# Kernel tuning notes

Hardware: AMD Instinct MI355X
Metric: run time of the kernel (lower is better)

The kernel has to match this reference:

```python
import jax, jax.numpy as jnp
import numpy as np

B, S, D = 4, 4096, 2048  # batch, seq, hidden
E, R, K = 8, 16, 2       # n_experts, rank, top_k


def setup_inputs() -> dict:
    key = jax.random.key(0)
    k1, k2, k3, k4 = jax.random.split(key, 4)
    x = jax.random.normal(k1, (B, S, D), dtype=jnp.float32)
    router_w = jax.random.normal(k2, (E, D), dtype=jnp.float32) * 0.02  # nn.Linear weight (out,in)
    experts_down = jax.random.normal(k3, (E, D, R), dtype=jnp.float32) * 0.01
    experts_up = jax.random.normal(k4, (E, R, D), dtype=jnp.float32) * 0.01
    return {"x": x, "router_w": router_w, "experts_down": experts_down, "experts_up": experts_up}


def reference(x, router_w, experts_down, experts_up):
    E_ = router_w.shape[0]
    # router sees detached x (torch: self.router(x.detach()))
    logits = jnp.einsum('bsd,ed->bse', jax.lax.stop_gradient(x), router_w)
    w, idx = jax.lax.top_k(logits, K)          # (B,S,K)
    w = jax.nn.softmax(w, axis=-1)
    # combined per-token, per-expert routing weight; zero for non-selected experts
    w_full = jnp.sum(jax.nn.one_hot(idx, E_, dtype=x.dtype) * w[..., None], axis=2)  # (B,S,E)
    # rank-space activations per expert: (B,S,E,R) -- small (R=16)
    h = jnp.einsum('bsd,edr->bser', x, experts_down)
    # fuse routing weight into rank space, then up-project and sum over experts
    out = x + jnp.einsum('bser,bse,erd->bsd', h, w_full, experts_up)
    return out
```

## Files before the change

kernel.cpp:

```cpp
#include <hip/hip_runtime.h>
#include <hip/hip_bf16.h>

#define MTOK 16384
#define DDIM 2048
#define NEXP 8
#define RNK 16
#define NC 128
#define NW 160
#define LOGIT0 128
#define KSPLIT 2
#define KLEN (DDIM / KSPLIT)
#define NT (KLEN / 64)

typedef __attribute__((ext_vector_type(8))) short bf16x8;
typedef __attribute__((ext_vector_type(4))) short short4v;
typedef __attribute__((ext_vector_type(4))) float f32x4;

typedef __attribute__((address_space(1))) const void gv_t;
typedef __attribute__((address_space(3))) void lv_t;

__device__ __forceinline__ short f2b(float f) {
  unsigned u = __float_as_uint(f);
  u += 0x7fffu + ((u >> 16) & 1u);
  return (short)(u >> 16);
}
__device__ __forceinline__ float b2f(short s) {
  return __uint_as_float(((unsigned)(unsigned short)s) << 16);
}

__global__ __launch_bounds__(256) void prep_k(const float* __restrict__ rw,
                                              const float* __restrict__ down,
                                              const float* __restrict__ up,
                                              short* __restrict__ WdT,
                                              short* __restrict__ UT) {
  int i = blockIdx.x * 256 + threadIdx.x;
  const int NWD = NW * DDIM;
  const int NUT = DDIM * NC;
  if (i < NWD) {
    int n = i / DDIM, k = i % DDIM;
    int s = (k >> 3) & 7;
    int src_k = (k & ~0x3F) | ((s ^ (n & 7)) << 3) | (k & 7);
    float v = 0.f;
    if (n < NC)             v = down[((n >> 4) * DDIM + src_k) * RNK + (n & 15)];
    else if (n < NC + NEXP) v = rw[(n - NC) * DDIM + src_k];
    WdT[i] = f2b(v);
  } else if (i < NWD + NUT) {
    int u = i - NWD;
    int d = u >> 7, c = u & 127;
    UT[u] = f2b(up[((c >> 4) * RNK + (c & 15)) * DDIM + d]);
  }
}

__global__ __launch_bounds__(256, 2) void gemm1_k(const float* __restrict__ X,
                                                  const short* __restrict__ WdT,
                                                  short* __restrict__ Hp) {
  __shared__ short Al[2][64][72];
  __shared__ short Bl[2][160 * 64];
  const int tid = threadIdx.x;
  const int lane = tid & 63;
  const int w = tid >> 6;
  const int gm0 = blockIdx.x * 64;
  const int ks = blockIdx.y;
  const int kb = ks * KLEN;
  const int wr = (w & 1) * 32;
  const int wc = (w >> 1) * 80;
  const int lr = lane & 15;
  const int lk = (lane >> 4) * 8;

  f32x4 acc[2][5];
#pragma unroll
  for (int m = 0; m < 2; ++m)
#pragma unroll
    for (int n = 0; n < 5; ++n) acc[m][n] = (f32x4){0.f, 0.f, 0.f, 0.f};

  float4 aR[4];

  auto loadA = [&](int k0) {
#pragma unroll
    for (int i2 = 0; i2 < 4; ++i2) {
      int f = tid + 256 * i2;
      int row = f >> 4, c4 = f & 15;
      aR[i2] = *(const float4*)(X + (size_t)(gm0 + row) * DDIM + k0 + c4 * 4);
    }
  };
  auto issueB = [&](int buf, int k0) {
#pragma unroll
    for (int j = 0; j < 5; ++j) {
      int u = (w * 5 + j) * 64 + lane;
      const short* g = WdT + (size_t)(u >> 3) * DDIM + k0 + (u & 7) * 8;
      short* l = &Bl[buf][(w * 5 + j) * 512];
      __builtin_amdgcn_global_load_lds((gv_t*)g, (lv_t*)l, 16, 0, 0);
    }
  };
  auto writeA = [&](int buf) {
#pragma unroll
    for (int i2 = 0; i2 < 4; ++i2) {
      int f = tid + 256 * i2;
      int row = f >> 4, c4 = f & 15;
      short4v v;
      v.x = f2b(aR[i2].x); v.y = f2b(aR[i2].y);
      v.z = f2b(aR[i2].z); v.w = f2b(aR[i2].w);
      *(short4v*)&Al[buf][row][c4 * 4] = v;
    }
  };
  auto compute = [&](int buf) {
#pragma unroll
    for (int kk2 = 0; kk2 < 2; ++kk2) {
      const int kk = kk2 * 32;
      bf16x8 a[2], b[5];
#pragma unroll
      for (int m = 0; m < 2; ++m)
        a[m] = *(const bf16x8*)&Al[buf][wr + m * 16 + lr][kk + lk];
#pragma unroll
      for (int n = 0; n < 5; ++n) {
        int row = wc + n * 16 + lr;
        int sl = ((kk >> 3) + (lane >> 4)) ^ (row & 7);
        b[n] = *(const bf16x8*)&Bl[buf][row * 64 + sl * 8];
      }
#pragma unroll
      for (int m = 0; m < 2; ++m)
#pragma unroll
        for (int n = 0; n < 5; ++n)
          acc[m][n] = __builtin_amdgcn_mfma_f32_16x16x32_bf16(a[m], b[n], acc[m][n], 0, 0, 0);
    }
  };

  loadA(kb);
  issueB(0, kb);
  writeA(0);
  __syncthreads();
  for (int t = 0; t < NT; ++t) {
    const int cur = t & 1, nxt = cur ^ 1;
    if (t + 1 < NT) {
      loadA(kb + (t + 1) * 64);
      issueB(nxt, kb + (t + 1) * 64);
    }
    compute(cur);
    if (t + 1 < NT) writeA(nxt);
    __syncthreads();
  }

  short* Hq = Hp + (size_t)ks * MTOK * NW;
  const int cr = (lane >> 4) * 4;
#pragma unroll
  for (int m = 0; m < 2; ++m)
#pragma unroll
    for (int n = 0; n < 5; ++n)
#pragma unroll
      for (int r = 0; r < 4; ++r) {
        int row = gm0 + wr + m * 16 + cr + r;
        int col = wc + n * 16 + lr;
        Hq[(size_t)row * NW + col] = f2b(acc[m][n][r]);
      }
}

__global__ __launch_bounds__(256) void route_k(const short* __restrict__ Hp,
                                               short* __restrict__ Hw) {
  __shared__ float wv[64][8];
  const int tid = threadIdx.x;
  const int t0 = blockIdx.x * 64;
  const short* H0 = Hp;
  const short* H1 = Hp + (size_t)MTOK * NW;
  if (tid < 64) {
    int t = t0 + tid;
    uint4 l0 = *(const uint4*)(H0 + (size_t)t * NW + LOGIT0);
    uint4 l1 = *(const uint4*)(H1 + (size_t)t * NW + LOGIT0);
    const short* p0 = (const short*)&l0;
    const short* p1 = (const short*)&l1;
    float b0 = -1e30f, b1 = -1e30f;
    int i0 = 0, i1 = 0;
#pragma unroll
    for (int e = 0; e < 8; ++e) {
      float v = b2f(p0[e]) + b2f(p1[e]);
      if (v > b0) { b1 = b0; i1 = i0; b0 = v; i0 = e; }
      else if (v > b1) { b1 = v; i1 = e; }
    }
    float ex = __expf(b1 - b0);
    float inv = 1.f / (1.f + ex);
#pragma unroll
    for (int e = 0; e < 8; ++e)
      wv[tid][e] = (e == i0) ? inv : ((e == i1) ? ex * inv : 0.f);
  }
  __syncthreads();
  const int t = tid >> 2, q = tid & 3;
  const short* a0 = H0 + (size_t)(t0 + t) * NW + q * 32;
  const short* a1 = H1 + (size_t)(t0 + t) * NW + q * 32;
  short* o = Hw + (size_t)(t0 + t) * NC + q * 32;
#pragma unroll
  for (int j = 0; j < 4; ++j) {
    uint4 v0 = *(const uint4*)(a0 + j * 8);
    uint4 v1 = *(const uint4*)(a1 + j * 8);
    const short* s0 = (const short*)&v0;
    const short* s1 = (const short*)&v1;
    short r[8];
    int cbase = q * 32 + j * 8;
#pragma unroll
    for (int e2 = 0; e2 < 8; ++e2) {
      float h = b2f(s0[e2]) + b2f(s1[e2]);
      r[e2] = f2b(h * wv[t][(cbase + e2) >> 4]);
    }
    *(uint4*)(o + j * 8) = *(uint4*)r;
  }
}

__global__ __launch_bounds__(256) void gemm2_k(const short* __restrict__ Hw,
                                               const short* __restrict__ UT,
                                               const float* __restrict__ X,
                                               float* __restrict__ Out) {
  __shared__ short Al[128][136];
  __shared__ short Bl[64][136];
  const int tid = threadIdx.x;
  const int lane = tid & 63;
  const int w = tid >> 6;
  const int gm0 = blockIdx.x * 128;
  const int n0 = blockIdx.y * 64;
  const int lr = lane & 15;
  const int lk = (lane >> 4) * 8;

#pragma unroll
  for (int i = 0; i < 8; ++i) {
    int f = tid + 256 * i;
    int row = f >> 4, c8 = f & 15;
    *(uint4*)&Al[row][c8 * 8] = *(const uint4*)(Hw + (size_t)(gm0 + row) * NC + c8 * 8);
  }
#pragma unroll
  for (int i = 0; i < 4; ++i) {
    int f = tid + 256 * i;
    int row = f >> 4, c8 = f & 15;
    *(uint4*)&Bl[row][c8 * 8] = *(const uint4*)(UT + (size_t)(n0 + row) * NC + c8 * 8);
  }
  __syncthreads();

  f32x4 acc[2][4];
#pragma unroll
  for (int m = 0; m < 2; ++m)
#pragma unroll
    for (int n = 0; n < 4; ++n) acc[m][n] = (f32x4){0.f, 0.f, 0.f, 0.f};

#pragma unroll
  for (int ks = 0; ks < 4; ++ks) {
    const int kk = ks * 32;
    bf16x8 a[2], b[4];
#pragma unroll
    for (int m = 0; m < 2; ++m) a[m] = *(const bf16x8*)&Al[w * 32 + m * 16 + lr][kk + lk];
#pragma unroll
    for (int n = 0; n < 4; ++n) b[n] = *(const bf16x8*)&Bl[n * 16 + lr][kk + lk];
#pragma unroll
    for (int m = 0; m < 2; ++m)
#pragma unroll
      for (int n = 0; n < 4; ++n)
        acc[m][n] = __builtin_amdgcn_mfma_f32_16x16x32_bf16(a[m], b[n], acc[m][n], 0, 0, 0);
  }

  const int cr = (lane >> 4) * 4;
#pragma unroll
  for (int m = 0; m < 2; ++m)
#pragma unroll
    for (int n = 0; n < 4; ++n)
#pragma unroll
      for (int r = 0; r < 4; ++r) {
        int row = gm0 + w * 32 + m * 16 + cr + r;
        int col = n0 + n * 16 + lr;
        size_t idx = (size_t)row * DDIM + col;
        Out[idx] = X[idx] + acc[m][n][r];
      }
}

extern "C" void kernel_launch(void* const* d_in, const int* in_sizes, int n_in,
                              void* d_out, int out_size, void* d_ws, size_t ws_size,
                              hipStream_t stream) {
  const float* x    = (const float*)d_in[0];
  const float* rw   = (const float*)d_in[1];
  const float* down = (const float*)d_in[2];
  const float* up   = (const float*)d_in[3];
  float* out = (float*)d_out;

  char* ws = (char*)d_ws;
  short* WdT = (short*)ws;
  short* UT  = (short*)(ws + 655360);
  short* Hp  = (short*)(ws + 1179648);
  short* Hw  = (short*)(ws + 11665408);

  prep_k<<<2304, 256, 0, stream>>>(rw, down, up, WdT, UT);
  gemm1_k<<<dim3(MTOK / 64, KSPLIT), 256, 0, stream>>>(x, WdT, Hp);
  route_k<<<MTOK / 64, 256, 0, stream>>>(Hp, Hw);
  gemm2_k<<<dim3(MTOK / 128, DDIM / 64), 256, 0, stream>>>(Hw, UT, x, out);
}
```

Before: 92.35 us.

## Fuse down-projection, routing and up-projection into one per-token-tile kernel

Replaces the three kernels (split-K down GEMM, routing, up GEMM) with a single kernel. Each block handles 32 tokens over the full K dimension, computes top-2 routing from the logit columns in shared memory, scales the rank activations, then runs the up-projection and residual add directly. This removes the global round trips for the partial H buffers and two launches. In exchange it drops split-K and uses smaller M tiles. The second stage reads UT fragments straight from global memory without LDS staging, and each block writes a full 32x2048 output tile, so the work per block becomes large and serialised.

```diff
diff --git a/kernel.cpp b/kernel.cpp
--- a/kernel.cpp
+++ b/kernel.cpp
@@ -7,10 +7,8 @@
 #define RNK 16
 #define NC 128
 #define NW 160
-#define LOGIT0 128
-#define KSPLIT 2
-#define KLEN (DDIM / KSPLIT)
-#define NT (KLEN / 64)
+#define BM 32
+#define NT2 (DDIM / 64)
 
 typedef __attribute__((ext_vector_type(8))) short bf16x8;
 typedef __attribute__((ext_vector_type(4))) short short4v;
@@ -23,9 +21,6 @@
   unsigned u = __float_as_uint(f);
   u += 0x7fffu + ((u >> 16) & 1u);
   return (short)(u >> 16);
-}
-__device__ __forceinline__ float b2f(short s) {
-  return __uint_as_float(((unsigned)(unsigned short)s) << 16);
 }
 
 __global__ __launch_bounds__(256) void prep_k(const float* __restrict__ rw,
@@ -51,33 +46,33 @@
   }
 }
 
-__global__ __launch_bounds__(256, 2) void gemm1_k(const float* __restrict__ X,
+__global__ __launch_bounds__(256, 2) void fused_k(const float* __restrict__ X,
                                                   const short* __restrict__ WdT,
-                                                  short* __restrict__ Hp) {
-  __shared__ short Al[2][64][72];
+                                                  const short* __restrict__ UT,
+                                                  float* __restrict__ Out) {
+  __shared__ short Al[2][BM][72];
   __shared__ short Bl[2][160 * 64];
+  __shared__ short HwS[BM][136];
+  __shared__ float lg[BM][8];
+  __shared__ float wv[BM][8];
   const int tid = threadIdx.x;
   const int lane = tid & 63;
   const int w = tid >> 6;
-  const int gm0 = blockIdx.x * 64;
-  const int ks = blockIdx.y;
-  const int kb = ks * KLEN;
-  const int wr = (w & 1) * 32;
+  const int gm0 = blockIdx.x * BM;
+  const int wr = (w & 1) * 16;
   const int wc = (w >> 1) * 80;
   const int lr = lane & 15;
   const int lk = (lane >> 4) * 8;
 
-  f32x4 acc[2][5];
-#pragma unroll
-  for (int m = 0; m < 2; ++m)
-#pragma unroll
-    for (int n = 0; n < 5; ++n) acc[m][n] = (f32x4){0.f, 0.f, 0.f, 0.f};
-
-  float4 aR[4];
+  f32x4 acc[5];
+#pragma unroll
+  for (int n = 0; n < 5; ++n) acc[n] = (f32x4){0.f, 0.f, 0.f, 0.f};
+
+  float4 aR[2];
 
   auto loadA = [&](int k0) {
 #pragma unroll
-    for (int i2 = 0; i2 < 4; ++i2) {
+    for (int i2 = 0; i2 < 2; ++i2) {
       int f = tid + 256 * i2;
       int row = f >> 4, c4 = f & 15;
       aR[i2] = *(const float4*)(X + (size_t)(gm0 + row) * DDIM + k0 + c4 * 4);
@@ -94,7 +89,7 @@
   };
   auto writeA = [&](int buf) {
 #pragma unroll
-    for (int i2 = 0; i2 < 4; ++i2) {
+    for (int i2 = 0; i2 < 2; ++i2) {
       int f = tid + 256 * i2;
       int row = f >> 4, c4 = f & 15;
       short4v v;
@@ -107,10 +102,8 @@
 #pragma unroll
     for (int kk2 = 0; kk2 < 2; ++kk2) {
       const int kk = kk2 * 32;
-      bf16x8 a[2], b[5];
-#pragma unroll
-      for (int m = 0; m < 2; ++m)
-        a[m] = *(const bf16x8*)&Al[buf][wr + m * 16 + lr][kk + lk];
+      bf16x8 a = *(const bf16x8*)&Al[buf][wr + lr][kk + lk];
+      bf16x8 b[5];
 #pragma unroll
       for (int n = 0; n < 5; ++n) {
         int row = wc + n * 16 + lr;
@@ -118,60 +111,38 @@
         b[n] = *(const bf16x8*)&Bl[buf][row * 64 + sl * 8];
       }
 #pragma unroll
-      for (int m = 0; m < 2; ++m)
-#pragma unroll
-        for (int n = 0; n < 5; ++n)
-          acc[m][n] = __builtin_amdgcn_mfma_f32_16x16x32_bf16(a[m], b[n], acc[m][n], 0, 0, 0);
-    }
-  };
-
-  loadA(kb);
-  issueB(0, kb);
+      for (int n = 0; n < 5; ++n)
+        acc[n] = __builtin_amdgcn_mfma_f32_16x16x32_bf16(a, b[n], acc[n], 0, 0, 0);
+    }
+  };
+
+  loadA(0);
+  issueB(0, 0);
   writeA(0);
   __syncthreads();
-  for (int t = 0; t < NT; ++t) {
+  for (int t = 0; t < NT2; ++t) {
     const int cur = t & 1, nxt = cur ^ 1;
-    if (t + 1 < NT) {
-      loadA(kb + (t + 1) * 64);
-      issueB(nxt, kb + (t + 1) * 64);
+    if (t + 1 < NT2) {
+      loadA((t + 1) * 64);
+      issueB(nxt, (t + 1) * 64);
     }
     compute(cur);
-    if (t + 1 < NT) writeA(nxt);
+    if (t + 1 < NT2) writeA(nxt);
     __syncthreads();
   }
 
-  short* Hq = Hp + (size_t)ks * MTOK * NW;
-  const int cr = (lane >> 4) * 4;
-#pragma unroll
-  for (int m = 0; m < 2; ++m)
-#pragma unroll
-    for (int n = 0; n < 5; ++n)
-#pragma unroll
-      for (int r = 0; r < 4; ++r) {
-        int row = gm0 + wr + m * 16 + cr + r;
-        int col = wc + n * 16 + lr;
-        Hq[(size_t)row * NW + col] = f2b(acc[m][n][r]);
-      }
-}
-
-__global__ __launch_bounds__(256) void route_k(const short* __restrict__ Hp,
-                                               short* __restrict__ Hw) {
-  __shared__ float wv[64][8];
-  const int tid = threadIdx.x;
-  const int t0 = blockIdx.x * 64;
-  const short* H0 = Hp;
-  const short* H1 = Hp + (size_t)MTOK * NW;
-  if (tid < 64) {
-    int t = t0 + tid;
-    uint4 l0 = *(const uint4*)(H0 + (size_t)t * NW + LOGIT0);
-    uint4 l1 = *(const uint4*)(H1 + (size_t)t * NW + LOGIT0);
-    const short* p0 = (const short*)&l0;
-    const short* p1 = (const short*)&l1;
+  if (wc == 80 && lr < 8) {
+#pragma unroll
+    for (int r = 0; r < 4; ++r)
+      lg[wr + (lane >> 4) * 4 + r][lr] = acc[3][r];
+  }
+  __syncthreads();
+  if (tid < BM) {
     float b0 = -1e30f, b1 = -1e30f;
     int i0 = 0, i1 = 0;
 #pragma unroll
     for (int e = 0; e < 8; ++e) {
-      float v = b2f(p0[e]) + b2f(p1[e]);
+      float v = lg[tid][e];
       if (v > b0) { b1 = b0; i1 = i0; b0 = v; i0 = e; }
       else if (v > b1) { b1 = v; i1 = e; }
     }
@@ -182,88 +153,56 @@
       wv[tid][e] = (e == i0) ? inv : ((e == i1) ? ex * inv : 0.f);
   }
   __syncthreads();
-  const int t = tid >> 2, q = tid & 3;
-  const short* a0 = H0 + (size_t)(t0 + t) * NW + q * 32;
-  const short* a1 = H1 + (size_t)(t0 + t) * NW + q * 32;
-  short* o = Hw + (size_t)(t0 + t) * NC + q * 32;
-#pragma unroll
-  for (int j = 0; j < 4; ++j) {
-    uint4 v0 = *(const uint4*)(a0 + j * 8);
-    uint4 v1 = *(const uint4*)(a1 + j * 8);
-    const short* s0 = (const short*)&v0;
-    const short* s1 = (const short*)&v1;
-    short r[8];
-    int cbase = q * 32 + j * 8;
-#pragma unroll
-    for (int e2 = 0; e2 < 8; ++e2) {
-      float h = b2f(s0[e2]) + b2f(s1[e2]);
-      r[e2] = f2b(h * wv[t][(cbase + e2) >> 4]);
-    }
-    *(uint4*)(o + j * 8) = *(uint4*)r;
-  }
-}
-
-__global__ __launch_bounds__(256) void gemm2_k(const short* __restrict__ Hw,
-                                               const short* __restrict__ UT,
-                                               const float* __restrict__ X,
-                                               float* __restrict__ Out) {
-  __shared__ short Al[128][136];
-  __shared__ short Bl[64][136];
-  const int tid = threadIdx.x;
-  const int lane = tid & 63;
-  const int w = tid >> 6;
-  const int gm0 = blockIdx.x * 128;
-  const int n0 = blockIdx.y * 64;
-  const int lr = lane & 15;
-  const int lk = (lane >> 4) * 8;
-
-#pragma unroll
-  for (int i = 0; i < 8; ++i) {
-    int f = tid + 256 * i;
-    int row = f >> 4, c8 = f & 15;
-    *(uint4*)&Al[row][c8 * 8] = *(const uint4*)(Hw + (size_t)(gm0 + row) * NC + c8 * 8);
-  }
-#pragma unroll
-  for (int i = 0; i < 4; ++i) {
-    int f = tid + 256 * i;
-    int row = f >> 4, c8 = f & 15;
-    *(uint4*)&Bl[row][c8 * 8] = *(const uint4*)(UT + (size_t)(n0 + row) * NC + c8 * 8);
-  }
-  __syncthreads();
-
-  f32x4 acc[2][4];
+
+  {
+    const int cmax = (wc == 0) ? 5 : 3;
+#pragma unroll
+    for (int n = 0; n < 5; ++n) {
+      if (n >= cmax) break;
+      int col = wc + n * 16 + lr;
+#pragma unroll
+      for (int r = 0; r < 4; ++r) {
+        int row = wr + (lane >> 4) * 4 + r;
+        HwS[row][col] = f2b(acc[n][r] * wv[row][col >> 4]);
+      }
+    }
+  }
+  __syncthreads();
+
+  bf16x8 af[2][4];
 #pragma unroll
   for (int m = 0; m < 2; ++m)
 #pragma unroll
-    for (int n = 0; n < 4; ++n) acc[m][n] = (f32x4){0.f, 0.f, 0.f, 0.f};
-
-#pragma unroll
-  for (int ks = 0; ks < 4; ++ks) {
-    const int kk = ks * 32;
-    bf16x8 a[2], b[4];
-#pragma unroll
-    for (int m = 0; m < 2; ++m) a[m] = *(const bf16x8*)&Al[w * 32 + m * 16 + lr][kk + lk];
-#pragma unroll
-    for (int n = 0; n < 4; ++n) b[n] = *(const bf16x8*)&Bl[n * 16 + lr][kk + lk];
-#pragma unroll
-    for (int m = 0; m < 2; ++m)
-#pragma unroll
-      for (int n = 0; n < 4; ++n)
-        acc[m][n] = __builtin_amdgcn_mfma_f32_16x16x32_bf16(a[m], b[n], acc[m][n], 0, 0, 0);
-  }
-
-  const int cr = (lane >> 4) * 4;
-#pragma unroll
-  for (int m = 0; m < 2; ++m)
-#pragma unroll
-    for (int n = 0; n < 4; ++n)
-#pragma unroll
-      for (int r = 0; r < 4; ++r) {
-        int row = gm0 + w * 32 + m * 16 + cr + r;
-        int col = n0 + n * 16 + lr;
-        size_t idx = (size_t)row * DDIM + col;
-        Out[idx] = X[idx] + acc[m][n][r];
-      }
+    for (int kc = 0; kc < 4; ++kc)
+      af[m][kc] = *(const bf16x8*)&HwS[m * 16 + lr][kc * 32 + lk];
+
+  const int ncol0 = w * 512;
+  for (int nb = 0; nb < 8; ++nb) {
+#pragma unroll
+    for (int nf = 0; nf < 4; ++nf) {
+      const int c0 = ncol0 + nb * 64 + nf * 16;
+      bf16x8 bfr[4];
+#pragma unroll
+      for (int kc = 0; kc < 4; ++kc)
+        bfr[kc] = *(const bf16x8*)(UT + (size_t)(c0 + lr) * NC + kc * 32 + lk);
+      f32x4 a2[2];
+#pragma unroll
+      for (int m = 0; m < 2; ++m) a2[m] = (f32x4){0.f, 0.f, 0.f, 0.f};
+#pragma unroll
+      for (int m = 0; m < 2; ++m)
+#pragma unroll
+        for (int kc = 0; kc < 4; ++kc)
+          a2[m] = __builtin_amdgcn_mfma_f32_16x16x32_bf16(af[m][kc], bfr[kc], a2[m], 0, 0, 0);
+#pragma unroll
+      for (int m = 0; m < 2; ++m)
+#pragma unroll
+        for (int r = 0; r < 4; ++r) {
+          int row = gm0 + m * 16 + (lane >> 4) * 4 + r;
+          size_t idx = (size_t)row * DDIM + c0 + lr;
+          Out[idx] = X[idx] + a2[m][r];
+        }
+    }
+  }
 }
 
 extern "C" void kernel_launch(void* const* d_in, const int* in_sizes, int n_in,
@@ -278,11 +217,7 @@
   char* ws = (char*)d_ws;
   short* WdT = (short*)ws;
   short* UT  = (short*)(ws + 655360);
-  short* Hp  = (short*)(ws + 1179648);
-  short* Hw  = (short*)(ws + 11665408);
 
   prep_k<<<2304, 256, 0, stream>>>(rw, down, up, WdT, UT);
-  gemm1_k<<<dim3(MTOK / 64, KSPLIT), 256, 0, stream>>>(x, WdT, Hp);
-  route_k<<<MTOK / 64, 256, 0, stream>>>(Hp, Hw);
-  gemm2_k<<<dim3(MTOK / 128, DDIM / 64), 256, 0, stream>>>(Hw, UT, x, out);
-}
+  fused_k<<<MTOK / BM, 256, 0, stream>>>(x, WdT, UT, out);
+}
```

New measurement: 105.4 us. +14.1%, slower.

## Read gemm1 B operand directly from global and stage gemm2 epilogue in LDS

Applied to the files above, without the earlier changes.

Removes the LDS staging of the down/router weight tile in gemm1 (and its XOR swizzle in the prep kernel), so MFMA B fragments are loaded straight from global memory, and raises the launch bound to 4 waves-per-EU with the smaller LDS footprint. The second GEMM's epilogue now writes accumulators to a padded LDS scratch and then performs float4-vectorised residual add and store instead of scalar strided writes. The intent is higher occupancy and coalesced output traffic, at the cost of gemm1 B reads hitting L2/global per MFMA step without explicit reuse through LDS.

```diff
diff --git a/kernel.cpp b/kernel.cpp
--- a/kernel.cpp
+++ b/kernel.cpp
@@ -16,9 +16,6 @@
 typedef __attribute__((ext_vector_type(4))) short short4v;
 typedef __attribute__((ext_vector_type(4))) float f32x4;
 
-typedef __attribute__((address_space(1))) const void gv_t;
-typedef __attribute__((address_space(3))) void lv_t;
-
 __device__ __forceinline__ short f2b(float f) {
   unsigned u = __float_as_uint(f);
   u += 0x7fffu + ((u >> 16) & 1u);
@@ -38,11 +35,9 @@
   const int NUT = DDIM * NC;
   if (i < NWD) {
     int n = i / DDIM, k = i % DDIM;
-    int s = (k >> 3) & 7;
-    int src_k = (k & ~0x3F) | ((s ^ (n & 7)) << 3) | (k & 7);
     float v = 0.f;
-    if (n < NC)             v = down[((n >> 4) * DDIM + src_k) * RNK + (n & 15)];
-    else if (n < NC + NEXP) v = rw[(n - NC) * DDIM + src_k];
+    if (n < NC)             v = down[((n >> 4) * DDIM + k) * RNK + (n & 15)];
+    else if (n < NC + NEXP) v = rw[(n - NC) * DDIM + k];
     WdT[i] = f2b(v);
   } else if (i < NWD + NUT) {
     int u = i - NWD;
@@ -51,11 +46,10 @@
   }
 }
 
-__global__ __launch_bounds__(256, 2) void gemm1_k(const float* __restrict__ X,
+__global__ __launch_bounds__(256, 4) void gemm1_k(const float* __restrict__ X,
                                                   const short* __restrict__ WdT,
                                                   short* __restrict__ Hp) {
   __shared__ short Al[2][64][72];
-  __shared__ short Bl[2][160 * 64];
   const int tid = threadIdx.x;
   const int lane = tid & 63;
   const int w = tid >> 6;
@@ -83,15 +77,6 @@
       aR[i2] = *(const float4*)(X + (size_t)(gm0 + row) * DDIM + k0 + c4 * 4);
     }
   };
-  auto issueB = [&](int buf, int k0) {
-#pragma unroll
-    for (int j = 0; j < 5; ++j) {
-      int u = (w * 5 + j) * 64 + lane;
-      const short* g = WdT + (size_t)(u >> 3) * DDIM + k0 + (u & 7) * 8;
-      short* l = &Bl[buf][(w * 5 + j) * 512];
-      __builtin_amdgcn_global_load_lds((gv_t*)g, (lv_t*)l, 16, 0, 0);
-    }
-  };
   auto writeA = [&](int buf) {
 #pragma unroll
     for (int i2 = 0; i2 < 4; ++i2) {
@@ -103,7 +88,7 @@
       *(short4v*)&Al[buf][row][c4 * 4] = v;
     }
   };
-  auto compute = [&](int buf) {
+  auto compute = [&](int buf, int k0) {
 #pragma unroll
     for (int kk2 = 0; kk2 < 2; ++kk2) {
       const int kk = kk2 * 32;
@@ -112,11 +97,8 @@
       for (int m = 0; m < 2; ++m)
         a[m] = *(const bf16x8*)&Al[buf][wr + m * 16 + lr][kk + lk];
 #pragma unroll
-      for (int n = 0; n < 5; ++n) {
-        int row = wc + n * 16 + lr;
-        int sl = ((kk >> 3) + (lane >> 4)) ^ (row & 7);
-        b[n] = *(const bf16x8*)&Bl[buf][row * 64 + sl * 8];
-      }
+      for (int n = 0; n < 5; ++n)
+        b[n] = *(const bf16x8*)(WdT + (size_t)(wc + n * 16 + lr) * DDIM + k0 + kk + lk);
 #pragma unroll
       for (int m = 0; m < 2; ++m)
 #pragma unroll
@@ -126,16 +108,12 @@
   };
 
   loadA(kb);
-  issueB(0, kb);
   writeA(0);
   __syncthreads();
   for (int t = 0; t < NT; ++t) {
     const int cur = t & 1, nxt = cur ^ 1;
-    if (t + 1 < NT) {
-      loadA(kb + (t + 1) * 64);
-      issueB(nxt, kb + (t + 1) * 64);
-    }
-    compute(cur);
+    if (t + 1 < NT) loadA(kb + (t + 1) * 64);
+    compute(cur, kb + t * 64);
     if (t + 1 < NT) writeA(nxt);
     __syncthreads();
   }
@@ -252,18 +230,26 @@
         acc[m][n] = __builtin_amdgcn_mfma_f32_16x16x32_bf16(a[m], b[n], acc[m][n], 0, 0, 0);
   }
 
+  float* eps = (float*)&Al[0][0] + w * 2176;
   const int cr = (lane >> 4) * 4;
 #pragma unroll
   for (int m = 0; m < 2; ++m)
 #pragma unroll
     for (int n = 0; n < 4; ++n)
 #pragma unroll
-      for (int r = 0; r < 4; ++r) {
-        int row = gm0 + w * 32 + m * 16 + cr + r;
-        int col = n0 + n * 16 + lr;
-        size_t idx = (size_t)row * DDIM + col;
-        Out[idx] = X[idx] + acc[m][n][r];
-      }
+      for (int r = 0; r < 4; ++r)
+        eps[(m * 16 + cr + r) * 68 + n * 16 + lr] = acc[m][n][r];
+
+#pragma unroll
+  for (int j = 0; j < 8; ++j) {
+    int c = lane + 64 * j;
+    int rl = c >> 4, c4 = c & 15;
+    float4 v = *(const float4*)&eps[rl * 68 + c4 * 4];
+    size_t idx = (size_t)(gm0 + w * 32 + rl) * DDIM + n0 + c4 * 4;
+    const float4 xv = *(const float4*)(X + idx);
+    v.x += xv.x; v.y += xv.y; v.z += xv.z; v.w += xv.w;
+    *(float4*)(Out + idx) = v;
+  }
 }
 
 extern "C" void kernel_launch(void* const* d_in, const int* in_sizes, int n_in,
```

Result: slower. 109.8 us (+18.9%).

## Halve gemm1 row tile and stage gemm2 epilogue through LDS for vector stores

Applied to the files above, without the earlier changes.

gemm1 now uses 32-row tiles instead of 64, doubling the grid and raising the occupancy hint to 3 blocks per CU. That trades reuse of the B tile (more WdT reloads per token) for more parallelism and fewer registers per wave. gemm2's epilogue now writes accumulators to LDS and then reads them back as float4, so the residual add and output stores are coalesced 16-byte accesses instead of scattered scalar ones. The LDS reuse in gemm2 depends on the Al buffer being large enough for each wave's 32x68 float region.

```diff
diff --git a/kernel.cpp b/kernel.cpp
--- a/kernel.cpp
+++ b/kernel.cpp
@@ -11,6 +11,7 @@
 #define KSPLIT 2
 #define KLEN (DDIM / KSPLIT)
 #define NT (KLEN / 64)
+#define BM1 32
 
 typedef __attribute__((ext_vector_type(8))) short bf16x8;
 typedef __attribute__((ext_vector_type(4))) short short4v;
@@ -51,33 +52,31 @@
   }
 }
 
-__global__ __launch_bounds__(256, 2) void gemm1_k(const float* __restrict__ X,
+__global__ __launch_bounds__(256, 3) void gemm1_k(const float* __restrict__ X,
                                                   const short* __restrict__ WdT,
                                                   short* __restrict__ Hp) {
-  __shared__ short Al[2][64][72];
+  __shared__ short Al[2][BM1][72];
   __shared__ short Bl[2][160 * 64];
   const int tid = threadIdx.x;
   const int lane = tid & 63;
   const int w = tid >> 6;
-  const int gm0 = blockIdx.x * 64;
+  const int gm0 = blockIdx.x * BM1;
   const int ks = blockIdx.y;
   const int kb = ks * KLEN;
-  const int wr = (w & 1) * 32;
+  const int wr = (w & 1) * 16;
   const int wc = (w >> 1) * 80;
   const int lr = lane & 15;
   const int lk = (lane >> 4) * 8;
 
-  f32x4 acc[2][5];
-#pragma unroll
-  for (int m = 0; m < 2; ++m)
-#pragma unroll
-    for (int n = 0; n < 5; ++n) acc[m][n] = (f32x4){0.f, 0.f, 0.f, 0.f};
-
-  float4 aR[4];
+  f32x4 acc[5];
+#pragma unroll
+  for (int n = 0; n < 5; ++n) acc[n] = (f32x4){0.f, 0.f, 0.f, 0.f};
+
+  float4 aR[2];
 
   auto loadA = [&](int k0) {
 #pragma unroll
-    for (int i2 = 0; i2 < 4; ++i2) {
+    for (int i2 = 0; i2 < 2; ++i2) {
       int f = tid + 256 * i2;
       int row = f >> 4, c4 = f & 15;
       aR[i2] = *(const float4*)(X + (size_t)(gm0 + row) * DDIM + k0 + c4 * 4);
@@ -94,7 +93,7 @@
   };
   auto writeA = [&](int buf) {
 #pragma unroll
-    for (int i2 = 0; i2 < 4; ++i2) {
+    for (int i2 = 0; i2 < 2; ++i2) {
       int f = tid + 256 * i2;
       int row = f >> 4, c4 = f & 15;
       short4v v;
@@ -107,10 +106,8 @@
 #pragma unroll
     for (int kk2 = 0; kk2 < 2; ++kk2) {
       const int kk = kk2 * 32;
-      bf16x8 a[2], b[5];
-#pragma unroll
-      for (int m = 0; m < 2; ++m)
-        a[m] = *(const bf16x8*)&Al[buf][wr + m * 16 + lr][kk + lk];
+      bf16x8 a = *(const bf16x8*)&Al[buf][wr + lr][kk + lk];
+      bf16x8 b[5];
 #pragma unroll
       for (int n = 0; n < 5; ++n) {
         int row = wc + n * 16 + lr;
@@ -118,10 +115,8 @@
         b[n] = *(const bf16x8*)&Bl[buf][row * 64 + sl * 8];
       }
 #pragma unroll
-      for (int m = 0; m < 2; ++m)
-#pragma unroll
-        for (int n = 0; n < 5; ++n)
-          acc[m][n] = __builtin_amdgcn_mfma_f32_16x16x32_bf16(a[m], b[n], acc[m][n], 0, 0, 0);
+      for (int n = 0; n < 5; ++n)
+        acc[n] = __builtin_amdgcn_mfma_f32_16x16x32_bf16(a, b[n], acc[n], 0, 0, 0);
     }
   };
 
@@ -143,15 +138,13 @@
   short* Hq = Hp + (size_t)ks * MTOK * NW;
   const int cr = (lane >> 4) * 4;
 #pragma unroll
-  for (int m = 0; m < 2; ++m)
-#pragma unroll
-    for (int n = 0; n < 5; ++n)
-#pragma unroll
-      for (int r = 0; r < 4; ++r) {
-        int row = gm0 + wr + m * 16 + cr + r;
-        int col = wc + n * 16 + lr;
-        Hq[(size_t)row * NW + col] = f2b(acc[m][n][r]);
-      }
+  for (int n = 0; n < 5; ++n)
+#pragma unroll
+    for (int r = 0; r < 4; ++r) {
+      int row = gm0 + wr + cr + r;
+      int col = wc + n * 16 + lr;
+      Hq[(size_t)row * NW + col] = f2b(acc[n][r]);
+    }
 }
 
 __global__ __launch_bounds__(256) void route_k(const short* __restrict__ Hp,
@@ -252,18 +245,26 @@
         acc[m][n] = __builtin_amdgcn_mfma_f32_16x16x32_bf16(a[m], b[n], acc[m][n], 0, 0, 0);
   }
 
+  float* eps = (float*)&Al[0][0] + w * 2176;
   const int cr = (lane >> 4) * 4;
 #pragma unroll
   for (int m = 0; m < 2; ++m)
 #pragma unroll
     for (int n = 0; n < 4; ++n)
 #pragma unroll
-      for (int r = 0; r < 4; ++r) {
-        int row = gm0 + w * 32 + m * 16 + cr + r;
-        int col = n0 + n * 16 + lr;
-        size_t idx = (size_t)row * DDIM + col;
-        Out[idx] = X[idx] + acc[m][n][r];
-      }
+      for (int r = 0; r < 4; ++r)
+        eps[(m * 16 + cr + r) * 68 + n * 16 + lr] = acc[m][n][r];
+
+#pragma unroll
+  for (int j = 0; j < 8; ++j) {
+    int c = lane + 64 * j;
+    int rl = c >> 4, c4 = c & 15;
+    float4 v = *(const float4*)&eps[rl * 68 + c4 * 4];
+    size_t idx = (size_t)(gm0 + w * 32 + rl) * DDIM + n0 + c4 * 4;
+    const float4 xv = *(const float4*)(X + idx);
+    v.x += xv.x; v.y += xv.y; v.z += xv.z; v.w += xv.w;
+    *(float4*)(Out + idx) = v;
+  }
 }
 
 extern "C" void kernel_launch(void* const* d_in, const int* in_sizes, int n_in,
@@ -282,7 +283,7 @@
   short* Hw  = (short*)(ws + 11665408);
 
   prep_k<<<2304, 256, 0, stream>>>(rw, down, up, WdT, UT);
-  gemm1_k<<<dim3(MTOK / 64, KSPLIT), 256, 0, stream>>>(x, WdT, Hp);
+  gemm1_k<<<dim3(MTOK / BM1, KSPLIT), 256, 0, stream>>>(x, WdT, Hp);
   route_k<<<MTOK / 64, 256, 0, stream>>>(Hp, Hw);
   gemm2_k<<<dim3(MTOK / 128, DDIM / 64), 256, 0, stream>>>(Hw, UT, x, out);
 }
```

Result: slower. 106.8 us (+15.7%).
